# Performance work log

Measured on AMD Instinct MI355X. Metric: run time of the kernel, lower is better.

The kernel has to match this reference:

```python
import jax, jax.numpy as jnp
import numpy as np

B, D, H1, H2, E, O = 32768, 256, 512, 256, 16, 64


def setup_inputs() -> dict:
    key = jax.random.key(0)
    ks = jax.random.split(key, 12)
    s = lambda fan_in: 1.0 / np.sqrt(fan_in)
    return {
        "x": jax.random.normal(ks[0], (B, D), dtype=jnp.float32),
        "gate_w": jax.random.normal(ks[1], (D, E), dtype=jnp.float32) * s(D),
        "gate_b": jnp.zeros((E,), dtype=jnp.float32),
        "W1": jax.random.normal(ks[2], (E, D, H1), dtype=jnp.float32) * s(D),
        "b1": jnp.zeros((E, H1), dtype=jnp.float32),
        "W2": jax.random.normal(ks[3], (E, H1, H2), dtype=jnp.float32) * s(H1),
        "b2": jnp.zeros((E, H2), dtype=jnp.float32),
        "W3": jax.random.normal(ks[4], (E, H2, O), dtype=jnp.float32) * s(H2),
        "b3": jnp.zeros((E, O), dtype=jnp.float32),
        "head_w": jax.random.normal(ks[5], (O, 1), dtype=jnp.float32) * s(O),
        "head_b": jnp.zeros((1,), dtype=jnp.float32),
    }


def reference(x, gate_w, gate_b, W1, b1, W2, b2, W3, b3, head_w, head_b):
    # gating: softmax over experts, [B, E]
    gates = jax.nn.softmax(x @ gate_w + gate_b, axis=-1)
    # all-expert dense MLP as batched GEMMs over leading expert axis
    h1 = jax.nn.relu(jnp.einsum('bd,edh->ebh', x, W1) + b1[:, None, :])   # [E,B,H1]
    h2 = jax.nn.relu(jnp.einsum('ebh,ehk->ebk', h1, W2) + b2[:, None, :])  # [E,B,H2]
    eo = jnp.einsum('ebk,eko->ebo', h2, W3) + b3[:, None, :]               # [E,B,O]
    # gated combination: sum_e gates[b,e] * eo[e,b,:]
    fused = jnp.einsum('be,ebo->bo', gates, eo)                            # [B,O]
    yts = (fused @ head_w + head_b)[:, 0]                                  # [B]
    return yts
```

## Files before the change

kernel.cpp:

```cpp
#include <hip/hip_runtime.h>

#define B_TOK 32768
#define D_IN  256
#define H1D   512
#define H2D   256
#define NE    16
#define NO    64
#define TK    128

typedef _Float16 half8 __attribute__((ext_vector_type(8)));
typedef _Float16 half4 __attribute__((ext_vector_type(4)));
typedef float   float4_t __attribute__((ext_vector_type(4)));

#define BARRIER_LGKM() do {                                   \
    __builtin_amdgcn_sched_barrier(0);                        \
    asm volatile("s_waitcnt lgkmcnt(0)" ::: "memory");        \
    __builtin_amdgcn_s_barrier();                             \
    __builtin_amdgcn_sched_barrier(0);                        \
  } while (0)

__global__ void prep_kernel(const float* __restrict__ W1, const float* __restrict__ W2,
                            const float* __restrict__ W3, const float* __restrict__ b3,
                            const float* __restrict__ hw, const float* __restrict__ gw,
                            _Float16* __restrict__ w1p, _Float16* __restrict__ w2p,
                            float* __restrict__ w3h, float* __restrict__ c3,
                            _Float16* __restrict__ gwp) {
  __shared__ _Float16 tile[32 * 516];
  const int blk = blockIdx.x;
  const int tid = threadIdx.x;

  if (blk < 128) {
    const int e = blk >> 3, kt = blk & 7;
    const float* src = W1 + ((size_t)(e * D_IN + kt * 32)) * H1D;
    #pragma unroll
    for (int it = 0; it < 16; ++it) {
      int idx = it * 256 + tid;
      int r = idx >> 7, c4 = idx & 127;
      float4_t v = *(const float4_t*)(src + (size_t)r * H1D + c4 * 4);
      half4 h;
      h[0] = (_Float16)v[0]; h[1] = (_Float16)v[1];
      h[2] = (_Float16)v[2]; h[3] = (_Float16)v[3];
      *(half4*)(tile + r * 516 + c4 * 4) = h;
    }
    __syncthreads();
    const int lane = tid & 63, wv = tid >> 6;
    #pragma unroll
    for (int it = 0; it < 8; ++it) {
      int ntg = it * 4 + wv;
      half8 v;
      #pragma unroll
      for (int j = 0; j < 8; ++j)
        v[j] = tile[((lane >> 4) * 8 + j) * 516 + ntg * 16 + (lane & 15)];
      *(half8*)(w1p + ((size_t)(((e * 32 + ntg) * 8 + kt) * 64 + lane)) * 8) = v;
    }
  } else if (blk < 384) {
    const int b2i = blk - 128;
    const int e = b2i >> 4, ktg = b2i & 15;
    const float* src = W2 + ((size_t)(e * H1D + ktg * 32)) * H2D;
    #pragma unroll
    for (int it = 0; it < 8; ++it) {
      int idx = it * 256 + tid;
      int r = idx >> 6, c4 = idx & 63;
      float4_t v = *(const float4_t*)(src + (size_t)r * H2D + c4 * 4);
      half4 h;
      h[0] = (_Float16)v[0]; h[1] = (_Float16)v[1];
      h[2] = (_Float16)v[2]; h[3] = (_Float16)v[3];
      *(half4*)(tile + r * 260 + c4 * 4) = h;
    }
    __syncthreads();
    const int lane = tid & 63, wv = tid >> 6;
    #pragma unroll
    for (int it = 0; it < 4; ++it) {
      int ntg = it * 4 + wv;
      half8 v;
      #pragma unroll
      for (int j = 0; j < 8; ++j)
        v[j] = tile[((lane >> 4) * 8 + j) * 260 + ntg * 16 + (lane & 15)];
      *(half8*)(w2p + ((size_t)(((e * 16 + ntg) * 16 + ktg) * 64 + lane)) * 8) = v;
    }
  } else if (blk < 401) {
    int t = (blk - 384) * 256 + tid;
    if (t < NE * H2D) {
      int e = t >> 8, h = t & 255;
      float s = 0.f;
      #pragma unroll
      for (int o = 0; o < NO; ++o) s = fmaf(W3[((size_t)(e * H2D + h)) * NO + o], hw[o], s);
      w3h[t] = s;
    } else if (t < NE * H2D + NE) {
      int e = t - NE * H2D;
      float s = 0.f;
      #pragma unroll
      for (int o = 0; o < NO; ++o) s = fmaf(b3[e * NO + o], hw[o], s);
      c3[e] = s;
    }
  } else {
    for (int t = tid; t < 512; t += 256) {
      int lane = t & 63;
      int kt   = t >> 6;
      int e  = lane & 15;
      int kb = kt * 32 + (lane >> 4) * 8;
      half8 v;
      #pragma unroll
      for (int j = 0; j < 8; ++j)
        v[j] = (_Float16)gw[(kb + j) * NE + e];
      *(half8*)(gwp + (size_t)t * 8) = v;
    }
  }
}

__global__ __launch_bounds__(512, 2) void moe_main(
    const float* __restrict__ x,
    const float* __restrict__ b1,
    const float* __restrict__ b2,
    const _Float16* __restrict__ w1p,
    const _Float16* __restrict__ w2p,
    const _Float16* __restrict__ gwp,
    const float* __restrict__ gb,
    const float* __restrict__ w3h,
    const float* __restrict__ c3,
    const float* __restrict__ head_b,
    float* __restrict__ out) {
  __shared__ _Float16 x_lds[64 * 512];
  __shared__ _Float16 h1c[64 * 512];
  __shared__ float g_lds[TK * 17];
  __shared__ float fin[8 * TK];

  const int tid  = threadIdx.x;
  const int w    = tid >> 6;
  const int lane = tid & 63;
  const int q    = lane >> 4;
  const int l16  = lane & 15;
  const int m0   = blockIdx.x * TK;

  const float4_t zero4 = (float4_t){0.f, 0.f, 0.f, 0.f};

  #pragma unroll
  for (int f = 0; f < 8; ++f) {
    const float* xr = x + (size_t)(m0 + w * 16 + l16) * D_IN + f * 32 + q * 8;
    float4_t v0 = *(const float4_t*)(xr);
    float4_t v1 = *(const float4_t*)(xr + 4);
    half8 h;
    h[0] = (_Float16)v0[0]; h[1] = (_Float16)v0[1];
    h[2] = (_Float16)v0[2]; h[3] = (_Float16)v0[3];
    h[4] = (_Float16)v1[0]; h[5] = (_Float16)v1[1];
    h[6] = (_Float16)v1[2]; h[7] = (_Float16)v1[3];
    *(half8*)(x_lds + (size_t)(w * 8 + f) * 512 + lane * 8) = h;
  }
  __syncthreads();

  {
    float gbv = gb[l16];
    float4_t lg = zero4;
    #pragma unroll
    for (int kt = 0; kt < 8; ++kt) {
      half8 xa = *(const half8*)(x_lds + (size_t)(w * 8 + kt) * 512 + lane * 8);
      half8 bfr = *(const half8*)(gwp + (size_t)kt * 512 + lane * 8);
      lg = __builtin_amdgcn_mfma_f32_16x16x32_f16(xa, bfr, lg, 0, 0, 0);
    }
    #pragma unroll
    for (int r = 0; r < 4; ++r) {
      float v = lg[r] + gbv;
      float m = v;
      m = fmaxf(m, __shfl_xor(m, 1));
      m = fmaxf(m, __shfl_xor(m, 2));
      m = fmaxf(m, __shfl_xor(m, 4));
      m = fmaxf(m, __shfl_xor(m, 8));
      float p = __expf(v - m);
      float s = p;
      s += __shfl_xor(s, 1);
      s += __shfl_xor(s, 2);
      s += __shfl_xor(s, 4);
      s += __shfl_xor(s, 8);
      g_lds[(w * 16 + q * 4 + r) * 17 + l16] = p / s;
    }
  }

  float yacc[8][4];
  #pragma unroll
  for (int mt = 0; mt < 8; ++mt)
    #pragma unroll
    for (int r = 0; r < 4; ++r) yacc[mt][r] = 0.f;

  for (int e = 0; e < NE; ++e) {
    float4_t h2[8][2];

    #pragma unroll
    for (int ch = 0; ch < 2; ++ch) {
      float4_t a1[2][8];

      const _Float16* w1e =
          w1p + ((size_t)((e * 32 + ch * 16 + w * 2) * 8)) * 512 + lane * 8;
      #pragma unroll
      for (int kt = 0; kt < 8; ++kt) {
        half8 wc[2];
        #pragma unroll
        for (int i = 0; i < 2; ++i)
          wc[i] = *(const half8*)(w1e + (size_t)(i * 8 + kt) * 512);
        half8 xb[8];
        #pragma unroll
        for (int nt = 0; nt < 8; ++nt)
          xb[nt] = *(const half8*)(x_lds + (size_t)(nt * 8 + kt) * 512 + lane * 8);
        #pragma unroll
        for (int i = 0; i < 2; ++i)
          #pragma unroll
          for (int nt = 0; nt < 8; ++nt)
            a1[i][nt] = __builtin_amdgcn_mfma_f32_16x16x32_f16(
                wc[i], xb[nt], (kt == 0) ? zero4 : a1[i][nt], 0, 0, 0);
      }

      #pragma unroll
      for (int i = 0; i < 2; ++i) {
        int colbase = ch * 256 + (w * 2 + i) * 16 + q * 4;
        float4_t bb = *(const float4_t*)(b1 + e * H1D + colbase);
        int qp = (i << 1) + (q >> 1);
        int fo = (qp * 16 + l16) * 8 + ((q & 1) << 2);
        #pragma unroll
        for (int nt = 0; nt < 8; ++nt) {
          half4 hv;
          #pragma unroll
          for (int r = 0; r < 4; ++r)
            hv[r] = (_Float16)fmaxf(a1[i][nt][r] + bb[r], 0.f);
          *(half4*)(h1c + (size_t)(nt * 8 + w) * 512 + fo) = hv;
        }
      }

      const _Float16* w2e =
          w2p + ((size_t)((e * 16 + w * 2) * 16 + ch * 8)) * 512 + lane * 8;
      half8 w2pre[2][4];
      #pragma unroll
      for (int j = 0; j < 2; ++j)
        #pragma unroll
        for (int kt = 0; kt < 4; ++kt)
          w2pre[j][kt] = *(const half8*)(w2e + (size_t)(j * 16 + kt) * 512);

      BARRIER_LGKM();

      #pragma unroll
      for (int kt = 0; kt < 4; ++kt) {
        half8 hac[8];
        #pragma unroll
        for (int mt = 0; mt < 8; ++mt)
          hac[mt] = *(const half8*)(h1c + (size_t)(mt * 8 + kt) * 512 + lane * 8);
        #pragma unroll
        for (int mt = 0; mt < 8; ++mt)
          #pragma unroll
          for (int j = 0; j < 2; ++j)
            h2[mt][j] = __builtin_amdgcn_mfma_f32_16x16x32_f16(
                hac[mt], w2pre[j][kt],
                (ch == 0 && kt == 0) ? zero4 : h2[mt][j], 0, 0, 0);
      }
      #pragma unroll
      for (int kt = 4; kt < 8; ++kt) {
        half8 w2c[2];
        #pragma unroll
        for (int j = 0; j < 2; ++j)
          w2c[j] = *(const half8*)(w2e + (size_t)(j * 16 + kt) * 512);
        half8 hac[8];
        #pragma unroll
        for (int mt = 0; mt < 8; ++mt)
          hac[mt] = *(const half8*)(h1c + (size_t)(mt * 8 + kt) * 512 + lane * 8);
        #pragma unroll
        for (int mt = 0; mt < 8; ++mt)
          #pragma unroll
          for (int j = 0; j < 2; ++j)
            h2[mt][j] = __builtin_amdgcn_mfma_f32_16x16x32_f16(
                hac[mt], w2c[j], h2[mt][j], 0, 0, 0);
      }

      if (ch == 1) {
        float b2v[2], w3v[2];
        #pragma unroll
        for (int j = 0; j < 2; ++j) {
          int n = (w * 2 + j) * 16 + l16;
          b2v[j] = b2[e * H2D + n];
          w3v[j] = w3h[e * H2D + n];
        }
        #pragma unroll
        for (int mt = 0; mt < 8; ++mt) {
          #pragma unroll
          for (int r = 0; r < 4; ++r) {
            float s = 0.f;
            #pragma unroll
            for (int j = 0; j < 2; ++j)
              s += fmaxf(h2[mt][j][r] + b2v[j], 0.f) * w3v[j];
            yacc[mt][r] += g_lds[(mt * 16 + q * 4 + r) * 17 + e] * s;
          }
        }
      }

      BARRIER_LGKM();
    }
  }

  #pragma unroll
  for (int mt = 0; mt < 8; ++mt) {
    #pragma unroll
    for (int r = 0; r < 4; ++r) {
      float v = yacc[mt][r];
      v += __shfl_xor(v, 1);
      v += __shfl_xor(v, 2);
      v += __shfl_xor(v, 4);
      v += __shfl_xor(v, 8);
      yacc[mt][r] = v;
    }
  }
  if (l16 == 0) {
    #pragma unroll
    for (int mt = 0; mt < 8; ++mt)
      #pragma unroll
      for (int r = 0; r < 4; ++r)
        fin[w * TK + mt * 16 + q * 4 + r] = yacc[mt][r];
  }
  __syncthreads();
  if (tid < TK) {
    float sum = 0.f;
    #pragma unroll
    for (int k = 0; k < 8; ++k) sum += fin[k * TK + tid];
    float gc = 0.f;
    #pragma unroll
    for (int e = 0; e < NE; ++e) gc += g_lds[tid * 17 + e] * c3[e];
    out[m0 + tid] = sum + gc + head_b[0];
  }
}

extern "C" void kernel_launch(void* const* d_in, const int* in_sizes, int n_in,
                              void* d_out, int out_size, void* d_ws, size_t ws_size,
                              hipStream_t stream) {
  const float* x      = (const float*)d_in[0];
  const float* gate_w = (const float*)d_in[1];
  const float* gate_b = (const float*)d_in[2];
  const float* W1     = (const float*)d_in[3];
  const float* b1     = (const float*)d_in[4];
  const float* W2     = (const float*)d_in[5];
  const float* b2     = (const float*)d_in[6];
  const float* W3     = (const float*)d_in[7];
  const float* b3     = (const float*)d_in[8];
  const float* head_w = (const float*)d_in[9];
  const float* head_b = (const float*)d_in[10];
  float* out = (float*)d_out;

  char* ws = (char*)d_ws;
  _Float16* w1p = (_Float16*)(ws);
  _Float16* w2p = (_Float16*)(ws + 4194304);
  _Float16* gwp = (_Float16*)(ws + 8388608);
  float*    w3h = (float*)(ws + 8396800);
  float*    c3  = (float*)(ws + 8413184);

  hipLaunchKernelGGL(prep_kernel, dim3(402), dim3(256), 0, stream,
                     W1, W2, W3, b3, head_w, gate_w, w1p, w2p, w3h, c3, gwp);
  hipLaunchKernelGGL(moe_main, dim3(B_TOK / TK), dim3(512), 0, stream,
                     x, b1, b2, w1p, w2p, gwp, gate_b, w3h, c3, head_b, out);
}
```

Baseline: 346.7 us.

## Pre-pack x into fp16 MFMA layout and software-pipeline H1/H2 stages with double-buffered LDS

After: 774.0 us. 123% more time.

```diff
diff --git a/kernel.cpp b/kernel.cpp
--- a/kernel.cpp
+++ b/kernel.cpp
@@ -19,18 +19,44 @@
     __builtin_amdgcn_sched_barrier(0);                        \
   } while (0)
 
-__global__ void prep_kernel(const float* __restrict__ W1, const float* __restrict__ W2,
-                            const float* __restrict__ W3, const float* __restrict__ b3,
-                            const float* __restrict__ hw, const float* __restrict__ gw,
-                            _Float16* __restrict__ w1p, _Float16* __restrict__ w2p,
-                            float* __restrict__ w3h, float* __restrict__ c3,
-                            _Float16* __restrict__ gwp) {
-  __shared__ _Float16 tile[32 * 516];
+__global__ void prep_kernel(const float* __restrict__ X, const float* __restrict__ W1,
+                            const float* __restrict__ W2, const float* __restrict__ W3,
+                            const float* __restrict__ b3, const float* __restrict__ hw,
+                            const float* __restrict__ gw,
+                            _Float16* __restrict__ xp, _Float16* __restrict__ w1p,
+                            _Float16* __restrict__ w2p, float* __restrict__ w3h,
+                            float* __restrict__ c3, _Float16* __restrict__ gwp) {
+  __shared__ _Float16 tile[64 * 260];
   const int blk = blockIdx.x;
   const int tid = threadIdx.x;
 
-  if (blk < 128) {
-    const int e = blk >> 3, kt = blk & 7;
+  if (blk < 512) {
+    const int t0 = blk * 64;
+    #pragma unroll
+    for (int it = 0; it < 16; ++it) {
+      int idx = it * 256 + tid;
+      int r = idx >> 6, c4 = idx & 63;
+      float4_t v = *(const float4_t*)(X + (size_t)(t0 + r) * D_IN + c4 * 4);
+      half4 h;
+      h[0] = (_Float16)v[0]; h[1] = (_Float16)v[1];
+      h[2] = (_Float16)v[2]; h[3] = (_Float16)v[3];
+      *(half4*)(tile + r * 260 + c4 * 4) = h;
+    }
+    __syncthreads();
+    const int lane = tid & 63, wv = tid >> 6;
+    #pragma unroll
+    for (int it = 0; it < 8; ++it) {
+      int f = it * 4 + wv;
+      int tt = f >> 3, kt = f & 7;
+      half8 v;
+      #pragma unroll
+      for (int j = 0; j < 8; ++j)
+        v[j] = tile[(tt * 16 + (lane & 15)) * 260 + kt * 32 + (lane >> 4) * 8 + j];
+      *(half8*)(xp + ((size_t)(((blk * 4 + tt) * 8 + kt) * 64 + lane)) * 8) = v;
+    }
+  } else if (blk < 640) {
+    const int b1i = blk - 512;
+    const int e = b1i >> 3, kt = b1i & 7;
     const float* src = W1 + ((size_t)(e * D_IN + kt * 32)) * H1D;
     #pragma unroll
     for (int it = 0; it < 16; ++it) {
@@ -53,8 +79,8 @@
         v[j] = tile[((lane >> 4) * 8 + j) * 516 + ntg * 16 + (lane & 15)];
       *(half8*)(w1p + ((size_t)(((e * 32 + ntg) * 8 + kt) * 64 + lane)) * 8) = v;
     }
-  } else if (blk < 384) {
-    const int b2i = blk - 128;
+  } else if (blk < 896) {
+    const int b2i = blk - 640;
     const int e = b2i >> 4, ktg = b2i & 15;
     const float* src = W2 + ((size_t)(e * H1D + ktg * 32)) * H2D;
     #pragma unroll
@@ -78,8 +104,8 @@
         v[j] = tile[((lane >> 4) * 8 + j) * 260 + ntg * 16 + (lane & 15)];
       *(half8*)(w2p + ((size_t)(((e * 16 + ntg) * 16 + ktg) * 64 + lane)) * 8) = v;
     }
-  } else if (blk < 401) {
-    int t = (blk - 384) * 256 + tid;
+  } else if (blk < 913) {
+    int t = (blk - 896) * 256 + tid;
     if (t < NE * H2D) {
       int e = t >> 8, h = t & 255;
       float s = 0.f;
@@ -109,7 +135,7 @@
 }
 
 __global__ __launch_bounds__(512, 2) void moe_main(
-    const float* __restrict__ x,
+    const _Float16* __restrict__ xp,
     const float* __restrict__ b1,
     const float* __restrict__ b2,
     const _Float16* __restrict__ w1p,
@@ -120,8 +146,7 @@
     const float* __restrict__ c3,
     const float* __restrict__ head_b,
     float* __restrict__ out) {
-  __shared__ _Float16 x_lds[64 * 512];
-  __shared__ _Float16 h1c[64 * 512];
+  __shared__ _Float16 h1c[2][64 * 512];
   __shared__ float g_lds[TK * 17];
   __shared__ float fin[8 * TK];
 
@@ -131,29 +156,16 @@
   const int q    = lane >> 4;
   const int l16  = lane & 15;
   const int m0   = blockIdx.x * TK;
+  const size_t bt16 = (size_t)blockIdx.x * 8;
 
   const float4_t zero4 = (float4_t){0.f, 0.f, 0.f, 0.f};
-
-  #pragma unroll
-  for (int f = 0; f < 8; ++f) {
-    const float* xr = x + (size_t)(m0 + w * 16 + l16) * D_IN + f * 32 + q * 8;
-    float4_t v0 = *(const float4_t*)(xr);
-    float4_t v1 = *(const float4_t*)(xr + 4);
-    half8 h;
-    h[0] = (_Float16)v0[0]; h[1] = (_Float16)v0[1];
-    h[2] = (_Float16)v0[2]; h[3] = (_Float16)v0[3];
-    h[4] = (_Float16)v1[0]; h[5] = (_Float16)v1[1];
-    h[6] = (_Float16)v1[2]; h[7] = (_Float16)v1[3];
-    *(half8*)(x_lds + (size_t)(w * 8 + f) * 512 + lane * 8) = h;
-  }
-  __syncthreads();
 
   {
     float gbv = gb[l16];
     float4_t lg = zero4;
     #pragma unroll
     for (int kt = 0; kt < 8; ++kt) {
-      half8 xa = *(const half8*)(x_lds + (size_t)(w * 8 + kt) * 512 + lane * 8);
+      half8 xa = *(const half8*)(xp + ((size_t)((bt16 + w) * 8 + kt)) * 512 + lane * 8);
       half8 bfr = *(const half8*)(gwp + (size_t)kt * 512 + lane * 8);
       lg = __builtin_amdgcn_mfma_f32_16x16x32_f16(xa, bfr, lg, 0, 0, 0);
     }
@@ -181,15 +193,19 @@
     #pragma unroll
     for (int r = 0; r < 4; ++r) yacc[mt][r] = 0.f;
 
-  for (int e = 0; e < NE; ++e) {
-    float4_t h2[8][2];
-
-    #pragma unroll
-    for (int ch = 0; ch < 2; ++ch) {
+  float4_t h2[8][2];
+  #pragma unroll
+  for (int mt = 0; mt < 8; ++mt)
+    #pragma unroll
+    for (int j = 0; j < 2; ++j) h2[mt][j] = zero4;
+
+  for (int c = 0; c <= 2 * NE; ++c) {
+    if (c < 2 * NE) {
+      const int e = c >> 1, ch = c & 1;
       float4_t a1[2][8];
-
       const _Float16* w1e =
           w1p + ((size_t)((e * 32 + ch * 16 + w * 2) * 8)) * 512 + lane * 8;
+      const _Float16* xpe = xp + (bt16 * 8) * 512 + lane * 8;
       #pragma unroll
       for (int kt = 0; kt < 8; ++kt) {
         half8 wc[2];
@@ -199,7 +215,7 @@
         half8 xb[8];
         #pragma unroll
         for (int nt = 0; nt < 8; ++nt)
-          xb[nt] = *(const half8*)(x_lds + (size_t)(nt * 8 + kt) * 512 + lane * 8);
+          xb[nt] = *(const half8*)(xpe + (size_t)(nt * 8 + kt) * 512);
         #pragma unroll
         for (int i = 0; i < 2; ++i)
           #pragma unroll
@@ -208,6 +224,7 @@
                 wc[i], xb[nt], (kt == 0) ? zero4 : a1[i][nt], 0, 0, 0);
       }
 
+      _Float16* hw_ = h1c[c & 1];
       #pragma unroll
       for (int i = 0; i < 2; ++i) {
         int colbase = ch * 256 + (w * 2 + i) * 16 + q * 4;
@@ -220,37 +237,18 @@
           #pragma unroll
           for (int r = 0; r < 4; ++r)
             hv[r] = (_Float16)fmaxf(a1[i][nt][r] + bb[r], 0.f);
-          *(half4*)(h1c + (size_t)(nt * 8 + w) * 512 + fo) = hv;
+          *(half4*)(hw_ + (size_t)(nt * 8 + w) * 512 + fo) = hv;
         }
       }
-
+    }
+
+    if (c > 0) {
+      const int e2 = (c - 1) >> 1, ch2 = (c - 1) & 1;
+      const _Float16* hr = h1c[(c - 1) & 1];
       const _Float16* w2e =
-          w2p + ((size_t)((e * 16 + w * 2) * 16 + ch * 8)) * 512 + lane * 8;
-      half8 w2pre[2][4];
-      #pragma unroll
-      for (int j = 0; j < 2; ++j)
-        #pragma unroll
-        for (int kt = 0; kt < 4; ++kt)
-          w2pre[j][kt] = *(const half8*)(w2e + (size_t)(j * 16 + kt) * 512);
-
-      BARRIER_LGKM();
-
-      #pragma unroll
-      for (int kt = 0; kt < 4; ++kt) {
-        half8 hac[8];
-        #pragma unroll
-        for (int mt = 0; mt < 8; ++mt)
-          hac[mt] = *(const half8*)(h1c + (size_t)(mt * 8 + kt) * 512 + lane * 8);
-        #pragma unroll
-        for (int mt = 0; mt < 8; ++mt)
-          #pragma unroll
-          for (int j = 0; j < 2; ++j)
-            h2[mt][j] = __builtin_amdgcn_mfma_f32_16x16x32_f16(
-                hac[mt], w2pre[j][kt],
-                (ch == 0 && kt == 0) ? zero4 : h2[mt][j], 0, 0, 0);
-      }
-      #pragma unroll
-      for (int kt = 4; kt < 8; ++kt) {
+          w2p + ((size_t)((e2 * 16 + w * 2) * 16 + ch2 * 8)) * 512 + lane * 8;
+      #pragma unroll
+      for (int kt = 0; kt < 8; ++kt) {
         half8 w2c[2];
         #pragma unroll
         for (int j = 0; j < 2; ++j)
@@ -258,7 +256,7 @@
         half8 hac[8];
         #pragma unroll
         for (int mt = 0; mt < 8; ++mt)
-          hac[mt] = *(const half8*)(h1c + (size_t)(mt * 8 + kt) * 512 + lane * 8);
+          hac[mt] = *(const half8*)(hr + (size_t)(mt * 8 + kt) * 512 + lane * 8);
         #pragma unroll
         for (int mt = 0; mt < 8; ++mt)
           #pragma unroll
@@ -267,13 +265,14 @@
                 hac[mt], w2c[j], h2[mt][j], 0, 0, 0);
       }
 
-      if (ch == 1) {
+      if ((c & 1) == 0) {
+        const int ef = e2;
         float b2v[2], w3v[2];
         #pragma unroll
         for (int j = 0; j < 2; ++j) {
           int n = (w * 2 + j) * 16 + l16;
-          b2v[j] = b2[e * H2D + n];
-          w3v[j] = w3h[e * H2D + n];
+          b2v[j] = b2[ef * H2D + n];
+          w3v[j] = w3h[ef * H2D + n];
         }
         #pragma unroll
         for (int mt = 0; mt < 8; ++mt) {
@@ -283,13 +282,17 @@
             #pragma unroll
             for (int j = 0; j < 2; ++j)
               s += fmaxf(h2[mt][j][r] + b2v[j], 0.f) * w3v[j];
-            yacc[mt][r] += g_lds[(mt * 16 + q * 4 + r) * 17 + e] * s;
+            yacc[mt][r] += g_lds[(mt * 16 + q * 4 + r) * 17 + ef] * s;
           }
         }
+        #pragma unroll
+        for (int mt = 0; mt < 8; ++mt)
+          #pragma unroll
+          for (int j = 0; j < 2; ++j) h2[mt][j] = zero4;
       }
-
-      BARRIER_LGKM();
-    }
+    }
+
+    BARRIER_LGKM();
   }
 
   #pragma unroll
@@ -345,9 +348,10 @@
   _Float16* gwp = (_Float16*)(ws + 8388608);
   float*    w3h = (float*)(ws + 8396800);
   float*    c3  = (float*)(ws + 8413184);
-
-  hipLaunchKernelGGL(prep_kernel, dim3(402), dim3(256), 0, stream,
-                     W1, W2, W3, b3, head_w, gate_w, w1p, w2p, w3h, c3, gwp);
+  _Float16* xp  = (_Float16*)(ws + 8413248);
+
+  hipLaunchKernelGGL(prep_kernel, dim3(914), dim3(256), 0, stream,
+                     x, W1, W2, W3, b3, head_w, gate_w, xp, w1p, w2p, w3h, c3, gwp);
   hipLaunchKernelGGL(moe_main, dim3(B_TOK / TK), dim3(512), 0, stream,
-                     x, b1, b2, w1p, w2p, gwp, gate_b, w3h, c3, head_b, out);
+                     xp, b1, b2, w1p, w2p, gwp, gate_b, w3h, c3, head_b, out);
 }
```
